# Kernel tuning notes

Measured on AMD Instinct MI355X. Metric: run time of the kernel, lower is better.

Reference implementation:

```python
import jax, jax.numpy as jnp
import numpy as np

EMB = 1024
HEADS = 16
HEAD_DIM = EMB // HEADS
FF = 4 * EMB
EPS = 1e-5


def setup_inputs() -> dict:
    key = jax.random.key(0)
    ks = jax.random.split(key, 16)
    s = 0.02
    return {
        "x": jax.random.normal(ks[0], (2, 2048, EMB), dtype=jnp.float32),
        "ln1_g": jnp.ones((EMB,), jnp.float32),
        "ln1_b": jnp.zeros((EMB,), jnp.float32),
        "Wq": jax.random.normal(ks[1], (EMB, EMB), jnp.float32) * s,
        "bq": jnp.zeros((EMB,), jnp.float32),
        "Wk": jax.random.normal(ks[2], (EMB, EMB), jnp.float32) * s,
        "bk": jnp.zeros((EMB,), jnp.float32),
        "Wv": jax.random.normal(ks[3], (EMB, EMB), jnp.float32) * s,
        "bv": jnp.zeros((EMB,), jnp.float32),
        "Wo": jax.random.normal(ks[4], (EMB, EMB), jnp.float32) * s,
        "bo": jnp.zeros((EMB,), jnp.float32),
        "ln2_g": jnp.ones((EMB,), jnp.float32),
        "ln2_b": jnp.zeros((EMB,), jnp.float32),
        "W1": jax.random.normal(ks[5], (EMB, FF), jnp.float32) * s,
        "b1": jnp.zeros((FF,), jnp.float32),
        "W2": jax.random.normal(ks[6], (FF, EMB), jnp.float32) * s,
        "b2": jnp.zeros((EMB,), jnp.float32),
    }


def _layernorm(x, g, b):
    mu = jnp.mean(x, axis=-1, keepdims=True)
    var = jnp.var(x, axis=-1, keepdims=True)
    return (x - mu) * jax.lax.rsqrt(var + EPS) * g + b


def _attention(x, Wq, bq, Wk, bk, Wv, bv, Wo, bo):
    B, T, C = x.shape
    # [B,T,C] -> [B,H,T,Dh]
    def split(y):
        return y.reshape(B, T, HEADS, HEAD_DIM).transpose(0, 2, 1, 3)
    Q = split(x @ Wq + bq)
    K = split(x @ Wk + bk)
    V = split(x @ Wv + bv)
    att = jnp.einsum("bhqd,bhkd->bhqk", Q, K) / np.sqrt(HEAD_DIM).astype(np.float32)
    causal = jnp.tril(jnp.ones((T, T), bool))
    att = jnp.where(causal, att, -jnp.inf)
    att = jax.nn.softmax(att, axis=-1)
    out = jnp.einsum("bhqk,bhkd->bhqd", att, V)
    out = out.transpose(0, 2, 1, 3).reshape(B, T, C)
    return out @ Wo + bo


def reference(x, ln1_g, ln1_b, Wq, bq, Wk, bk, Wv, bv, Wo, bo,
              ln2_g, ln2_b, W1, b1, W2, b2):
    # dropout is identity in eval mode
    x = x + _attention(_layernorm(x, ln1_g, ln1_b), Wq, bq, Wk, bk, Wv, bv, Wo, bo)
    h = _layernorm(x, ln2_g, ln2_b)
    h = jax.nn.gelu(h @ W1 + b1, approximate=False) @ W2 + b2
    return x + h
```

## Files before the change

### kernel.cpp

```cpp
#include <hip/hip_runtime.h>
#include <hip/hip_bf16.h>

typedef __attribute__((ext_vector_type(4))) float f32x4;
typedef __attribute__((ext_vector_type(8))) short bf16x8;
typedef unsigned int u32;
typedef unsigned short u16;

#define GASP __attribute__((address_space(1)))
#define LASP __attribute__((address_space(3)))

__device__ __forceinline__ u16 f2bf(float f) {
  u32 u = __float_as_uint(f);
  return (u16)((u + 0x7fffu + ((u >> 16) & 1u)) >> 16);
}

__device__ __forceinline__ u32 cvtpk(float lo, float hi) {
  u32 r;
  asm("v_cvt_pk_bf16_f32 %0, %1, %2" : "=v"(r) : "v"(lo), "v"(hi));
  return r;
}

__device__ __forceinline__ void gl_lds16(const void* g, void* l) {
  __builtin_amdgcn_global_load_lds((const GASP u32*)g, (LASP u32*)l, 16, 0, 0);
}

struct CastArgs {
  const float* s[6];
  u16* d[6];
};

__global__ __launch_bounds__(256) void cast_w(CastArgs a) {
  int bid = blockIdx.x;
  int w, t, K, N, kshift;
  if (bid < 4096)      { w = bid >> 10; t = bid & 1023; K = 1024; N = 1024; kshift = 5; }
  else if (bid < 8192) { w = 4; t = bid - 4096; K = 1024; N = 4096; kshift = 5; }
  else                 { w = 5; t = bid - 8192; K = 4096; N = 1024; kshift = 7; }
  int tk = t & ((1 << kshift) - 1);
  int tn = t >> kshift;
  int k0 = tk << 5, n0 = tn << 5;
  const float* src = a.s[w];
  u16* dst = a.d[w];
  __shared__ u16 tile[32][36];
  int r = threadIdx.x >> 3, c0 = (threadIdx.x & 7) << 2;
  float4 v = *(const float4*)&src[(size_t)(k0 + r) * N + n0 + c0];
  tile[c0 + 0][r] = f2bf(v.x);
  tile[c0 + 1][r] = f2bf(v.y);
  tile[c0 + 2][r] = f2bf(v.z);
  tile[c0 + 3][r] = f2bf(v.w);
  __syncthreads();
  ushort4 o;
  o.x = tile[r][c0 + 0];
  o.y = tile[r][c0 + 1];
  o.z = tile[r][c0 + 2];
  o.w = tile[r][c0 + 3];
  *(ushort4*)&dst[(size_t)(n0 + r) * K + k0 + c0] = o;
}

__global__ __launch_bounds__(256) void ln_k(const float* __restrict__ x, const float* __restrict__ g,
                                            const float* __restrict__ b, u16* __restrict__ out) {
  int row = blockIdx.x;
  int tid = threadIdx.x;
  float4 v = *(const float4*)&x[(size_t)row * 1024 + tid * 4];
  float s = v.x + v.y + v.z + v.w;
  float ss = v.x * v.x + v.y * v.y + v.z * v.z + v.w * v.w;
#pragma unroll
  for (int o = 32; o >= 1; o >>= 1) {
    s += __shfl_xor(s, o, 64);
    ss += __shfl_xor(ss, o, 64);
  }
  __shared__ float red[8];
  int wv = tid >> 6;
  if ((tid & 63) == 0) { red[wv] = s; red[wv + 4] = ss; }
  __syncthreads();
  s = red[0] + red[1] + red[2] + red[3];
  ss = red[4] + red[5] + red[6] + red[7];
  float mu = s * (1.0f / 1024.0f);
  float var = ss * (1.0f / 1024.0f) - mu * mu;
  float rstd = rsqrtf(var + 1e-5f);
  float4 gv = *(const float4*)&g[tid * 4];
  float4 bv = *(const float4*)&b[tid * 4];
  ushort4 o4;
  o4.x = f2bf((v.x - mu) * rstd * gv.x + bv.x);
  o4.y = f2bf((v.y - mu) * rstd * gv.y + bv.y);
  o4.z = f2bf((v.z - mu) * rstd * gv.z + bv.z);
  o4.w = f2bf((v.w - mu) * rstd * gv.w + bv.w);
  *(ushort4*)&out[(size_t)row * 1024 + tid * 4] = o4;
}

template <int MODE>
__global__ __launch_bounds__(512, 2) void gemm_256(
    const u16* __restrict__ A, const u16* __restrict__ Bt,
    const float* __restrict__ bias0, const float* __restrict__ bias1, const float* __restrict__ bias2,
    void* outp, int rm, int rn, int xn, int M, int N, int K) {
  __shared__ __align__(16) u16 As[4][128 * 64];
  __shared__ __align__(16) u16 Bs[4][128 * 64];
  char* asB = (char*)As;
  char* bsB = (char*)Bs;
  const int tid = threadIdx.x;
  const int w = tid >> 6, lane = tid & 63;
  const int xcd = blockIdx.x & 7, idx = blockIdx.x >> 3;
  const int mt = (xcd / xn) * rm + (idx % rm);
  const int nt = (xcd % xn) * rn + (idx / rm);
  const int m0 = mt << 8, n0 = nt << 8;

  const int rA = tid >> 3;
  const int csw = ((tid & 7) ^ (rA & 7)) * 8;
  const u16* pA = A + (size_t)(m0 + rA) * K + csw;
  const u16* pB = Bt + (size_t)(n0 + rA) * K + csw;
  const int dstOff = tid * 16;

#define STG_A(kt, h, d_) do {                                            \
    const u16* s_ = pA + (size_t)((h) * 128) * K + (size_t)(kt) * 64;    \
    char* l_ = asB + ((d_) * 2 + (h)) * 16384 + dstOff;                  \
    gl_lds16(s_, l_);                                                    \
    gl_lds16(s_ + (size_t)64 * K, l_ + 8192);                            \
  } while (0)
#define STG_B(kt, h, d_) do {                                            \
    const u16* s_ = pB + (size_t)((h) * 128) * K + (size_t)(kt) * 64;    \
    char* l_ = bsB + ((d_) * 2 + (h)) * 16384 + dstOff;                  \
    gl_lds16(s_, l_);                                                    \
    gl_lds16(s_ + (size_t)64 * K, l_ + 8192);                            \
  } while (0)

  const int wr = w >> 2, wc = w & 3;
  const int g = lane >> 4, qi = lane & 15;

  int aOff[8][2], bOff[4][2];
#pragma unroll
  for (int mm = 0; mm < 8; ++mm) {
    int row = mm * 16 + qi;
#pragma unroll
    for (int ks = 0; ks < 2; ++ks)
      aOff[mm][ks] = row * 128 + (((ks * 4 + g) ^ (qi & 7)) << 4);
  }
#pragma unroll
  for (int nn = 0; nn < 4; ++nn) {
    int rowb = (wc & 1) * 64 + nn * 16 + qi;
#pragma unroll
    for (int ks = 0; ks < 2; ++ks)
      bOff[nn][ks] = rowb * 128 + (((ks * 4 + g) ^ (qi & 7)) << 4);
  }

  f32x4 acc[8][4];
#pragma unroll
  for (int i = 0; i < 8; ++i)
#pragma unroll
    for (int j = 0; j < 4; ++j) acc[i][j] = f32x4{0.f, 0.f, 0.f, 0.f};

#define MFMA16(MB, A00, A01, A10, A11) do {                                              \
    __builtin_amdgcn_s_setprio(1);                                                       \
    acc[(MB)][0] = __builtin_amdgcn_mfma_f32_16x16x32_bf16(A00, bv[0][0], acc[(MB)][0], 0, 0, 0); \
    acc[(MB)][1] = __builtin_amdgcn_mfma_f32_16x16x32_bf16(A00, bv[1][0], acc[(MB)][1], 0, 0, 0); \
    acc[(MB)][2] = __builtin_amdgcn_mfma_f32_16x16x32_bf16(A00, bv[2][0], acc[(MB)][2], 0, 0, 0); \
    acc[(MB)][3] = __builtin_amdgcn_mfma_f32_16x16x32_bf16(A00, bv[3][0], acc[(MB)][3], 0, 0, 0); \
    acc[(MB) + 1][0] = __builtin_amdgcn_mfma_f32_16x16x32_bf16(A10, bv[0][0], acc[(MB) + 1][0], 0, 0, 0); \
    acc[(MB) + 1][1] = __builtin_amdgcn_mfma_f32_16x16x32_bf16(A10, bv[1][0], acc[(MB) + 1][1], 0, 0, 0); \
    acc[(MB) + 1][2] = __builtin_amdgcn_mfma_f32_16x16x32_bf16(A10, bv[2][0], acc[(MB) + 1][2], 0, 0, 0); \
    acc[(MB) + 1][3] = __builtin_amdgcn_mfma_f32_16x16x32_bf16(A10, bv[3][0], acc[(MB) + 1][3], 0, 0, 0); \
    acc[(MB)][0] = __builtin_amdgcn_mfma_f32_16x16x32_bf16(A01, bv[0][1], acc[(MB)][0], 0, 0, 0); \
    acc[(MB)][1] = __builtin_amdgcn_mfma_f32_16x16x32_bf16(A01, bv[1][1], acc[(MB)][1], 0, 0, 0); \
    acc[(MB)][2] = __builtin_amdgcn_mfma_f32_16x16x32_bf16(A01, bv[2][1], acc[(MB)][2], 0, 0, 0); \
    acc[(MB)][3] = __builtin_amdgcn_mfma_f32_16x16x32_bf16(A01, bv[3][1], acc[(MB)][3], 0, 0, 0); \
    acc[(MB) + 1][0] = __builtin_amdgcn_mfma_f32_16x16x32_bf16(A11, bv[0][1], acc[(MB) + 1][0], 0, 0, 0); \
    acc[(MB) + 1][1] = __builtin_amdgcn_mfma_f32_16x16x32_bf16(A11, bv[1][1], acc[(MB) + 1][1], 0, 0, 0); \
    acc[(MB) + 1][2] = __builtin_amdgcn_mfma_f32_16x16x32_bf16(A11, bv[2][1], acc[(MB) + 1][2], 0, 0, 0); \
    acc[(MB) + 1][3] = __builtin_amdgcn_mfma_f32_16x16x32_bf16(A11, bv[3][1], acc[(MB) + 1][3], 0, 0, 0); \
    __builtin_amdgcn_s_setprio(0);                                                       \
  } while (0)

#define RDA(dst0, dst1, MB)                                          \
    bf16x8 dst0##0 = *(const bf16x8*)(asB + aTB + aOff[(MB)][0]);     \
    bf16x8 dst0##1 = *(const bf16x8*)(asB + aTB + aOff[(MB)][1]);     \
    bf16x8 dst1##0 = *(const bf16x8*)(asB + aTB + aOff[(MB) + 1][0]); \
    bf16x8 dst1##1 = *(const bf16x8*)(asB + aTB + aOff[(MB) + 1][1]);

  const int T = K >> 6;
  STG_A(0, 0, 0); STG_A(0, 1, 0);
  STG_B(0, 0, 0); STG_B(0, 1, 0);
  asm volatile("s_waitcnt vmcnt(0)" ::: "memory");
  __builtin_amdgcn_s_barrier();

  for (int t = 0; t < T; ++t) {
    const int d = t & 1;
    const int aTB = (d * 2 + wr) * 16384;
    const int bTB = (d * 2 + (wc >> 1)) * 16384;
    bf16x8 bv[4][2];
#pragma unroll
    for (int nn = 0; nn < 4; ++nn) {
      bv[nn][0] = *(const bf16x8*)(bsB + bTB + bOff[nn][0]);
      bv[nn][1] = *(const bf16x8*)(bsB + bTB + bOff[nn][1]);
    }
    RDA(p0a, p0b, 0);
    if (t + 1 < T) STG_A(t + 1, 0, d ^ 1);
    MFMA16(0, p0a0, p0a1, p0b0, p0b1);
    RDA(p1a, p1b, 2);
    if (t + 1 < T) STG_A(t + 1, 1, d ^ 1);
    MFMA16(2, p1a0, p1a1, p1b0, p1b1);
    RDA(p2a, p2b, 4);
    if (t + 1 < T) STG_B(t + 1, 0, d ^ 1);
    MFMA16(4, p2a0, p2a1, p2b0, p2b1);
    RDA(p3a, p3b, 6);
    if (t + 1 < T) STG_B(t + 1, 1, d ^ 1);
    MFMA16(6, p3a0, p3a1, p3b0, p3b1);
    asm volatile("" ::: "memory");
    if (t + 1 < T) { asm volatile("s_waitcnt vmcnt(0)" ::: "memory"); }
    __builtin_amdgcn_s_barrier();
  }
#undef MFMA16
#undef RDA
#undef STG_A
#undef STG_B

  const int ci = lane & 15;
#pragma unroll
  for (int mm = 0; mm < 8; ++mm) {
#pragma unroll
    for (int nn = 0; nn < 4; ++nn) {
      int colb = n0 + wc * 64 + nn * 16 + ci;
      int rowbase = m0 + wr * 128 + mm * 16 + 4 * g;
      f32x4 c = acc[mm][nn];
      if constexpr (MODE == 2) {
        int sel = colb >> 10;
        int cc = colb & 1023;
        const float* bp = sel == 0 ? bias0 : (sel == 1 ? bias1 : bias2);
        float bb = bp[cc];
        int h = cc >> 6, dd = cc & 63;
        int b_ = rowbase >> 11, tt = rowbase & 2047;
        if (sel == 2) {
          u16* op = (u16*)outp + 2ull * (4096ull * 1024ull);
          ushort4 o4;
          o4.x = f2bf(c[0] + bb);
          o4.y = f2bf(c[1] + bb);
          o4.z = f2bf(c[2] + bb);
          o4.w = f2bf(c[3] + bb);
          *(ushort4*)&op[((size_t)(b_ * 16 + h) * 64 + dd) * 2048 + tt] = o4;
        } else {
          float scale = (sel == 0) ? 0.125f : 1.0f;
          u16* op = (u16*)outp + (size_t)sel * (4096ull * 1024ull);
#pragma unroll
          for (int r = 0; r < 4; ++r)
            op[((size_t)(b_ * 16 + h) * 2048 + tt + r) * 64 + dd] = f2bf((c[r] + bb) * scale);
        }
      } else {
        float bb = bias0[colb];
#pragma unroll
        for (int r = 0; r < 4; ++r) {
          float v = c[r] + bb;
          float gl = 0.5f * v * (1.0f + erff(v * 0.70710678118654752f));
          ((u16*)outp)[(size_t)(rowbase + r) * N + colb] = f2bf(gl);
        }
      }
    }
  }
}

__global__ __launch_bounds__(512) void gemm_sk(
    const u16* __restrict__ A, const u16* __restrict__ Bt,
    const float* __restrict__ bias0, float* __restrict__ outp,
    const float* __restrict__ res, int M, int N, int K) {
  __shared__ __align__(16) union SM {
    struct { u16 As[2][4][128 * 32]; u16 Bs[2][4][128 * 32]; } t;
    float red[16][4][4][64];
  } sm;
  const int tid = threadIdx.x;
  const int w8 = tid >> 6, lane = tid & 63;
  const int gg = w8 >> 2, wl = w8 & 3;
  const int m0 = blockIdx.y << 7, n0 = blockIdx.x << 7;

  char* asB = (char*)sm.t.As[gg];
  char* bsB = (char*)sm.t.Bs[gg];
  const u16* aS[2];
  const u16* bS[2];
#pragma unroll
  for (int i = 0; i < 2; ++i) {
    int p = wl * 2048 + i * 1024 + lane * 16;
    int r = p >> 6;
    int cl = ((p >> 4) & 3) ^ ((r >> 1) & 3);
    aS[i] = A + (size_t)(m0 + r) * K + gg * 32 + cl * 8;
    bS[i] = Bt + (size_t)(n0 + r) * K + gg * 32 + cl * 8;
  }
  f32x4 acc[4][4];
#pragma unroll
  for (int i = 0; i < 4; ++i)
#pragma unroll
    for (int j = 0; j < 4; ++j) acc[i][j] = f32x4{0.f, 0.f, 0.f, 0.f};

  const int wr = wl >> 1, wc = wl & 1;
  int aOff[4], bOff[4];
#pragma unroll
  for (int mm = 0; mm < 4; ++mm) {
    int rowa = wr * 64 + mm * 16 + (lane & 15);
    aOff[mm] = rowa * 64 + (((lane >> 4) ^ ((rowa >> 1) & 3)) << 4);
    int rowb = wc * 64 + mm * 16 + (lane & 15);
    bOff[mm] = rowb * 64 + (((lane >> 4) ^ ((rowb >> 1) & 3)) << 4);
  }

  gl_lds16(aS[0], asB + wl * 2048);
  gl_lds16(aS[1], asB + wl * 2048 + 1024);
  gl_lds16(bS[0], bsB + wl * 2048);
  gl_lds16(bS[1], bsB + wl * 2048 + 1024);
  if (K > 64) {
    gl_lds16(aS[0] + 64, asB + 8192 + wl * 2048);
    gl_lds16(aS[1] + 64, asB + 8192 + wl * 2048 + 1024);
    gl_lds16(bS[0] + 64, bsB + 8192 + wl * 2048);
    gl_lds16(bS[1] + 64, bsB + 8192 + wl * 2048 + 1024);
  }
  if (K > 128) {
    gl_lds16(aS[0] + 128, asB + 16384 + wl * 2048);
    gl_lds16(aS[1] + 128, asB + 16384 + wl * 2048 + 1024);
    gl_lds16(bS[0] + 128, bsB + 16384 + wl * 2048);
    gl_lds16(bS[1] + 128, bsB + 16384 + wl * 2048 + 1024);
  }
  int buf = 0;
  for (int ks = 0; ks < K; ks += 64) {
    const int rem = ((K - ks) >> 6) - 1;
    if (rem >= 2)      { asm volatile("s_waitcnt vmcnt(8)" ::: "memory"); }
    else if (rem == 1) { asm volatile("s_waitcnt vmcnt(4)" ::: "memory"); }
    else               { asm volatile("s_waitcnt vmcnt(0)" ::: "memory"); }
    __builtin_amdgcn_s_barrier();
    asm volatile("" ::: "memory");
    if (ks + 192 < K) {
      const int nb = ((buf + 3) & 3) * 8192;
      gl_lds16(aS[0] + ks + 192, asB + nb + wl * 2048);
      gl_lds16(aS[1] + ks + 192, asB + nb + wl * 2048 + 1024);
      gl_lds16(bS[0] + ks + 192, bsB + nb + wl * 2048);
      gl_lds16(bS[1] + ks + 192, bsB + nb + wl * 2048 + 1024);
    }
    const int tb = buf * 8192;
    bf16x8 av[4], bv[4];
#pragma unroll
    for (int mm = 0; mm < 4; ++mm) av[mm] = *(const bf16x8*)(asB + tb + aOff[mm]);
#pragma unroll
    for (int nn = 0; nn < 4; ++nn) bv[nn] = *(const bf16x8*)(bsB + tb + bOff[nn]);
#pragma unroll
    for (int mm = 0; mm < 4; ++mm)
#pragma unroll
      for (int nn = 0; nn < 4; ++nn)
        acc[mm][nn] = __builtin_amdgcn_mfma_f32_16x16x32_bf16(av[mm], bv[nn], acc[mm][nn], 0, 0, 0);
    buf = (buf + 1) & 3;
  }

  __syncthreads();
  if (gg == 1) {
#pragma unroll
    for (int mm = 0; mm < 4; ++mm)
#pragma unroll
      for (int nn = 0; nn < 4; ++nn)
#pragma unroll
        for (int r = 0; r < 4; ++r) sm.red[mm * 4 + nn][r][wl][lane] = acc[mm][nn][r];
  }
  __syncthreads();
  if (gg == 0) {
    const int g = lane >> 4, ci = lane & 15;
#pragma unroll
    for (int mm = 0; mm < 4; ++mm) {
#pragma unroll
      for (int nn = 0; nn < 4; ++nn) {
        int colb = n0 + wc * 64 + nn * 16 + ci;
        int rowbase = m0 + wr * 64 + mm * 16 + 4 * g;
        float bb = bias0[colb];
#pragma unroll
        for (int r = 0; r < 4; ++r) {
          size_t idx = (size_t)(rowbase + r) * N + colb;
          outp[idx] = acc[mm][nn][r] + sm.red[mm * 4 + nn][r][wl][lane] + bb + res[idx];
        }
      }
    }
  }
}

__global__ __launch_bounds__(512) void attn_k(const u16* __restrict__ Q, const u16* __restrict__ Kg,
                                              const u16* __restrict__ Vt, u16* __restrict__ O) {
  __shared__ __align__(16) u16 Ks[2][4][64 * 64];
  __shared__ __align__(16) u16 Vs[2][4][64 * 64];
  const int bx = blockIdx.y;
  const int bh = blockIdx.x;
  const int tid = threadIdx.x, w = tid >> 6, lane = tid & 63;
  const int g = lane >> 4, qi = lane & 15;
  const u16* Qb = Q + (size_t)bh * 2048 * 64;
  const u16* Kb = Kg + (size_t)bh * 2048 * 64;
  const u16* Vtb = Vt + (size_t)bh * 64 * 2048;

  const int rS = tid >> 3, cS = tid & 7;
  const int csw = (cS ^ (rS & 7)) * 8;
  const u16* srcK = Kb + (size_t)rS * 64 + csw;
  const u16* srcV = Vtb + (size_t)rS * 2048 + csw;
  char* ksB = (char*)Ks;
  char* vsB = (char*)Vs;
  const int dstOff = tid * 16;

  int koff[4][2], voff[4][2];
#pragma unroll
  for (int t = 0; t < 4; ++t) {
    int row = 16 * t + qi;
#pragma unroll
    for (int h = 0; h < 2; ++h) koff[t][h] = row * 128 + (((4 * h + g) ^ (qi & 7)) << 4);
#pragma unroll
    for (int kt = 0; kt < 2; ++kt) voff[t][kt] = row * 128 + (((4 * kt + g) ^ (qi & 7)) << 4);
  }

  const int b_ = bh >> 4, hh = bh & 15;
  u32* Ou = (u32*)O;

  for (int job = 0; job < 2; ++job) {
    const int qt = job ? bx : 15 - bx;
    const int qmin = qt * 128 + w * 16;
    const int qrow = qmin + qi;
    const int qmaxw = qmin + 15;

    bf16x8 qf[2];
#pragma unroll
    for (int h = 0; h < 2; ++h)
      qf[h] = *(const bf16x8*)(Qb + (size_t)qrow * 64 + h * 32 + g * 8);

    f32x4 acc[4];
#pragma unroll
    for (int dt = 0; dt < 4; ++dt) acc[dt] = f32x4{0.f, 0.f, 0.f, 0.f};
    float m = -1e30f, lsum = 0.0f;

    __syncthreads();
#pragma unroll
    for (int j = 0; j < 4; ++j) {
      gl_lds16(srcK + (size_t)j * 4096, ksB + j * 8192 + dstOff);
      gl_lds16(srcV + (size_t)j * 64, vsB + j * 8192 + dstOff);
    }

    const int nsteps = 2 * qt + 2;
    const int quads = (nsteps + 3) >> 2;
    int ph = 0;
    for (int ss = 0; ss < quads; ++ss) {
      __syncthreads();
      if (ss + 1 < quads) {
        const int nb = (ph ^ 1) * 32768;
#pragma unroll
        for (int j = 0; j < 4; ++j) {
          const int sj = 4 * ss + 4 + j;
          gl_lds16(srcK + (size_t)sj * 4096, ksB + nb + j * 8192 + dstOff);
          gl_lds16(srcV + (size_t)sj * 64, vsB + nb + j * 8192 + dstOff);
        }
      }
#pragma unroll
      for (int j = 0; j < 4; ++j) {
        const int s = 4 * ss + j;
        const int kv0 = s * 64;
        if (kv0 <= qmaxw) {
          const int tb = ph * 32768 + j * 8192;
          f32x4 st[4];
          __builtin_amdgcn_s_setprio(1);
#pragma unroll
          for (int t = 0; t < 4; ++t) {
            st[t] = f32x4{0.f, 0.f, 0.f, 0.f};
#pragma unroll
            for (int h = 0; h < 2; ++h) {
              bf16x8 kf = *(const bf16x8*)(ksB + tb + koff[t][h]);
              st[t] = __builtin_amdgcn_mfma_f32_16x16x32_bf16(kf, qf[h], st[t], 0, 0, 0);
            }
          }
          __builtin_amdgcn_s_setprio(0);
          float pvv[4][4];
          float tmax = -1e30f;
          if (kv0 + 63 > qmin) {
#pragma unroll
            for (int t = 0; t < 4; ++t)
#pragma unroll
              for (int r = 0; r < 4; ++r) {
                int key = kv0 + 16 * t + 4 * g + r;
                float sv = st[t][r];
                sv = (key <= qrow) ? sv : -1e30f;
                pvv[t][r] = sv;
                tmax = fmaxf(tmax, sv);
              }
          } else {
#pragma unroll
            for (int t = 0; t < 4; ++t)
#pragma unroll
              for (int r = 0; r < 4; ++r) {
                float sv = st[t][r];
                pvv[t][r] = sv;
                tmax = fmaxf(tmax, sv);
              }
          }
          tmax = fmaxf(tmax, __shfl_xor(tmax, 16, 64));
          tmax = fmaxf(tmax, __shfl_xor(tmax, 32, 64));
          if (!__all(tmax <= m + 8.0f)) {
            float mn = fmaxf(m, tmax);
            float corr = __expf(m - mn);
            lsum *= corr;
#pragma unroll
            for (int dt = 0; dt < 4; ++dt)
#pragma unroll
              for (int r = 0; r < 4; ++r) acc[dt][r] *= corr;
            m = mn;
          }
          float tsum = 0.f;
#pragma unroll
          for (int t = 0; t < 4; ++t)
#pragma unroll
            for (int r = 0; r < 4; ++r) {
              float e = __expf(pvv[t][r] - m);
              pvv[t][r] = e;
              tsum += e;
            }
          tsum += __shfl_xor(tsum, 16, 64);
          tsum += __shfl_xor(tsum, 32, 64);
          lsum += tsum;
          u32 pk[4][2], ex[4][2];
#pragma unroll
          for (int t = 0; t < 4; ++t)
#pragma unroll
            for (int p = 0; p < 2; ++p) {
              u32 v = cvtpk(pvv[t][2 * p], pvv[t][2 * p + 1]);
              pk[t][p] = v;
              ex[t][p] = (u32)__shfl_xor((int)v, 16, 64);
            }
          const bool ge = (g & 1) == 0;
          const bool G0 = (g >> 1) == 0;
          const bool innr = (g == 0) || (g == 3);
          u32 mm_[4][4];
#pragma unroll
          for (int t = 0; t < 4; ++t) {
            mm_[t][0] = ge ? pk[t][0] : ex[t][0];
            mm_[t][1] = ge ? pk[t][1] : ex[t][1];
            mm_[t][2] = ge ? ex[t][0] : pk[t][0];
            mm_[t][3] = ge ? ex[t][1] : pk[t][1];
          }
          union Frag { u32 u[4]; bf16x8 v; } f0, f1;
#pragma unroll
          for (int i = 0; i < 4; ++i) {
            u32 sel0 = G0 ? mm_[1][i] : mm_[0][i];
            u32 sel1 = G0 ? mm_[3][i] : mm_[2][i];
            u32 sw0 = (u32)__shfl_xor((int)sel0, 32, 64);
            u32 sw1 = (u32)__shfl_xor((int)sel1, 32, 64);
            u32 own0 = G0 ? mm_[0][i] : mm_[1][i];
            u32 own1 = G0 ? mm_[2][i] : mm_[3][i];
            f0.u[i] = innr ? own0 : sw0;
            f1.u[i] = innr ? own1 : sw1;
          }
          __builtin_amdgcn_s_setprio(1);
#pragma unroll
          for (int dt = 0; dt < 4; ++dt) {
            bf16x8 vfa = *(const bf16x8*)(vsB + tb + voff[dt][0]);
            acc[dt] = __builtin_amdgcn_mfma_f32_16x16x32_bf16(vfa, f0.v, acc[dt], 0, 0, 0);
            bf16x8 vfb = *(const bf16x8*)(vsB + tb + voff[dt][1]);
            acc[dt] = __builtin_amdgcn_mfma_f32_16x16x32_bf16(vfb, f1.v, acc[dt], 0, 0, 0);
          }
          __builtin_amdgcn_s_setprio(0);
        }
      }
      ph ^= 1;
    }

    float rl = 1.0f / lsum;
    size_t rowq = (size_t)(b_ * 2048 + qrow);
#pragma unroll
    for (int dt = 0; dt < 4; ++dt) {
#pragma unroll
      for (int rp = 0; rp < 2; ++rp) {
        u16 lo = f2bf(acc[dt][rp * 2] * rl);
        u16 hi = f2bf(acc[dt][rp * 2 + 1] * rl);
        u32 pkd = (u32)lo | ((u32)hi << 16);
        size_t off = rowq * 1024 + hh * 64 + dt * 16 + 4 * g + rp * 2;
        Ou[off >> 1] = pkd;
      }
    }
  }
}

extern "C" void kernel_launch(void* const* d_in, const int* in_sizes, int n_in,
                              void* d_out, int out_size, void* d_ws, size_t ws_size,
                              hipStream_t stream) {
  const float* x    = (const float*)d_in[0];
  const float* ln1g = (const float*)d_in[1];
  const float* ln1b = (const float*)d_in[2];
  const float* Wq   = (const float*)d_in[3];
  const float* bq   = (const float*)d_in[4];
  const float* Wk   = (const float*)d_in[5];
  const float* bk   = (const float*)d_in[6];
  const float* Wv   = (const float*)d_in[7];
  const float* bv   = (const float*)d_in[8];
  const float* Wo   = (const float*)d_in[9];
  const float* bo   = (const float*)d_in[10];
  const float* ln2g = (const float*)d_in[11];
  const float* ln2b = (const float*)d_in[12];
  const float* W1   = (const float*)d_in[13];
  const float* b1   = (const float*)d_in[14];
  const float* W2   = (const float*)d_in[15];
  const float* b2   = (const float*)d_in[16];

  char* ws = (char*)d_ws;
  const size_t MB = 1ull << 20;
  u16* WqT = (u16*)(ws + 0 * MB);
  u16* WkT = (u16*)(ws + 2 * MB);
  u16* WvT = (u16*)(ws + 4 * MB);
  u16* WoT = (u16*)(ws + 6 * MB);
  u16* W1T = (u16*)(ws + 8 * MB);
  u16* W2T = (u16*)(ws + 16 * MB);
  u16* XN  = (u16*)(ws + 24 * MB);
  u16* Qb  = (u16*)(ws + 32 * MB);
  u16* Kb  = (u16*)(ws + 40 * MB);
  u16* Vtb = (u16*)(ws + 48 * MB);
  u16* Ob  = (u16*)(ws + 56 * MB);
  u16* Gb  = (u16*)(ws + 32 * MB);

  CastArgs ca;
  ca.s[0] = Wq; ca.s[1] = Wk; ca.s[2] = Wv; ca.s[3] = Wo; ca.s[4] = W1; ca.s[5] = W2;
  ca.d[0] = WqT; ca.d[1] = WkT; ca.d[2] = WvT; ca.d[3] = WoT; ca.d[4] = W1T; ca.d[5] = W2T;
  cast_w<<<12288, 256, 0, stream>>>(ca);

  ln_k<<<4096, 256, 0, stream>>>(x, ln1g, ln1b, XN);

  gemm_256<2><<<192, 512, 0, stream>>>(XN, WqT, bq, bk, bv, Qb, 4, 6, 2, 4096, 3072, 1024);

  attn_k<<<dim3(32, 8), 512, 0, stream>>>(Qb, Kb, Vtb, Ob);

  gemm_sk<<<dim3(8, 32), 512, 0, stream>>>(Ob, WoT, bo, (float*)d_out, x, 4096, 1024, 1024);

  ln_k<<<4096, 256, 0, stream>>>((const float*)d_out, ln2g, ln2b, XN);

  gemm_256<3><<<256, 512, 0, stream>>>(XN, W1T, b1, nullptr, nullptr, Gb, 8, 4, 4, 4096, 4096, 1024);

  gemm_sk<<<dim3(8, 32), 512, 0, stream>>>(Gb, W2T, b2, (float*)d_out, (const float*)d_out, 4096, 1024, 4096);
}
```

Baseline: 226.8 us.

## Template GEMM on N-tile width, use 256x192 tiles for QKV projection

The 256-wide GEMM is parameterized on the N tile width, with a simpler LDS layout and warp-to-column mapping (each warp covers BN/4 columns). The QKV projection now uses 256x192 tiles, launching 256 blocks instead of 192, which better fills the GPU's compute units (256 on MI355X) and balances across XCDs. The trade-off is less B-tile reuse per block, and the warp mapping changes for the FFN GEMM too.

```diff
diff --git a/kernel.cpp b/kernel.cpp
--- a/kernel.cpp
+++ b/kernel.cpp
@@ -87,13 +87,15 @@
   *(ushort4*)&out[(size_t)row * 1024 + tid * 4] = o4;
 }
 
-template <int MODE>
+template <int MODE, int BN>
 __global__ __launch_bounds__(512, 2) void gemm_256(
     const u16* __restrict__ A, const u16* __restrict__ Bt,
     const float* __restrict__ bias0, const float* __restrict__ bias1, const float* __restrict__ bias2,
     void* outp, int rm, int rn, int xn, int M, int N, int K) {
-  __shared__ __align__(16) u16 As[4][128 * 64];
-  __shared__ __align__(16) u16 Bs[4][128 * 64];
+  constexpr int NN = BN / 64;
+  constexpr int BB = BN * 128;
+  __shared__ __align__(16) u16 As[2][256 * 64];
+  __shared__ __align__(16) u16 Bs[2][BN * 64];
   char* asB = (char*)As;
   char* bsB = (char*)Bs;
   const int tid = threadIdx.x;
@@ -101,7 +103,7 @@
   const int xcd = blockIdx.x & 7, idx = blockIdx.x >> 3;
   const int mt = (xcd / xn) * rm + (idx % rm);
   const int nt = (xcd % xn) * rn + (idx / rm);
-  const int m0 = mt << 8, n0 = nt << 8;
+  const int m0 = mt << 8, n0 = nt * BN;
 
   const int rA = tid >> 3;
   const int csw = ((tid & 7) ^ (rA & 7)) * 8;
@@ -109,62 +111,46 @@
   const u16* pB = Bt + (size_t)(n0 + rA) * K + csw;
   const int dstOff = tid * 16;
 
-#define STG_A(kt, h, d_) do {                                            \
-    const u16* s_ = pA + (size_t)((h) * 128) * K + (size_t)(kt) * 64;    \
-    char* l_ = asB + ((d_) * 2 + (h)) * 16384 + dstOff;                  \
-    gl_lds16(s_, l_);                                                    \
-    gl_lds16(s_ + (size_t)64 * K, l_ + 8192);                            \
-  } while (0)
-#define STG_B(kt, h, d_) do {                                            \
-    const u16* s_ = pB + (size_t)((h) * 128) * K + (size_t)(kt) * 64;    \
-    char* l_ = bsB + ((d_) * 2 + (h)) * 16384 + dstOff;                  \
-    gl_lds16(s_, l_);                                                    \
-    gl_lds16(s_ + (size_t)64 * K, l_ + 8192);                            \
-  } while (0)
+#define STG_A(kt, j) gl_lds16(pA + (size_t)((j) * 64) * K + (size_t)(kt) * 64, asB + aNB + (j) * 8192 + dstOff)
+#define STG_B(kt, j) gl_lds16(pB + (size_t)((j) * 64) * K + (size_t)(kt) * 64, bsB + bNB + (j) * 8192 + dstOff)
 
   const int wr = w >> 2, wc = w & 3;
   const int g = lane >> 4, qi = lane & 15;
 
-  int aOff[8][2], bOff[4][2];
+  int aOff[8][2], bOff[NN][2];
 #pragma unroll
   for (int mm = 0; mm < 8; ++mm) {
-    int row = mm * 16 + qi;
+    int row = wr * 128 + mm * 16 + qi;
 #pragma unroll
     for (int ks = 0; ks < 2; ++ks)
       aOff[mm][ks] = row * 128 + (((ks * 4 + g) ^ (qi & 7)) << 4);
   }
 #pragma unroll
-  for (int nn = 0; nn < 4; ++nn) {
-    int rowb = (wc & 1) * 64 + nn * 16 + qi;
+  for (int nn = 0; nn < NN; ++nn) {
+    int rowb = wc * (BN / 4) + nn * 16 + qi;
 #pragma unroll
     for (int ks = 0; ks < 2; ++ks)
       bOff[nn][ks] = rowb * 128 + (((ks * 4 + g) ^ (qi & 7)) << 4);
   }
 
-  f32x4 acc[8][4];
+  f32x4 acc[8][NN];
 #pragma unroll
   for (int i = 0; i < 8; ++i)
 #pragma unroll
-    for (int j = 0; j < 4; ++j) acc[i][j] = f32x4{0.f, 0.f, 0.f, 0.f};
-
-#define MFMA16(MB, A00, A01, A10, A11) do {                                              \
+    for (int j = 0; j < NN; ++j) acc[i][j] = f32x4{0.f, 0.f, 0.f, 0.f};
+
+#define PAIR(MB, A00, A01, A10, A11) do {                                                \
     __builtin_amdgcn_s_setprio(1);                                                       \
-    acc[(MB)][0] = __builtin_amdgcn_mfma_f32_16x16x32_bf16(A00, bv[0][0], acc[(MB)][0], 0, 0, 0); \
-    acc[(MB)][1] = __builtin_amdgcn_mfma_f32_16x16x32_bf16(A00, bv[1][0], acc[(MB)][1], 0, 0, 0); \
-    acc[(MB)][2] = __builtin_amdgcn_mfma_f32_16x16x32_bf16(A00, bv[2][0], acc[(MB)][2], 0, 0, 0); \
-    acc[(MB)][3] = __builtin_amdgcn_mfma_f32_16x16x32_bf16(A00, bv[3][0], acc[(MB)][3], 0, 0, 0); \
-    acc[(MB) + 1][0] = __builtin_amdgcn_mfma_f32_16x16x32_bf16(A10, bv[0][0], acc[(MB) + 1][0], 0, 0, 0); \
-    acc[(MB) + 1][1] = __builtin_amdgcn_mfma_f32_16x16x32_bf16(A10, bv[1][0], acc[(MB) + 1][1], 0, 0, 0); \
-    acc[(MB) + 1][2] = __builtin_amdgcn_mfma_f32_16x16x32_bf16(A10, bv[2][0], acc[(MB) + 1][2], 0, 0, 0); \
-    acc[(MB) + 1][3] = __builtin_amdgcn_mfma_f32_16x16x32_bf16(A10, bv[3][0], acc[(MB) + 1][3], 0, 0, 0); \
-    acc[(MB)][0] = __builtin_amdgcn_mfma_f32_16x16x32_bf16(A01, bv[0][1], acc[(MB)][0], 0, 0, 0); \
-    acc[(MB)][1] = __builtin_amdgcn_mfma_f32_16x16x32_bf16(A01, bv[1][1], acc[(MB)][1], 0, 0, 0); \
-    acc[(MB)][2] = __builtin_amdgcn_mfma_f32_16x16x32_bf16(A01, bv[2][1], acc[(MB)][2], 0, 0, 0); \
-    acc[(MB)][3] = __builtin_amdgcn_mfma_f32_16x16x32_bf16(A01, bv[3][1], acc[(MB)][3], 0, 0, 0); \
-    acc[(MB) + 1][0] = __builtin_amdgcn_mfma_f32_16x16x32_bf16(A11, bv[0][1], acc[(MB) + 1][0], 0, 0, 0); \
-    acc[(MB) + 1][1] = __builtin_amdgcn_mfma_f32_16x16x32_bf16(A11, bv[1][1], acc[(MB) + 1][1], 0, 0, 0); \
-    acc[(MB) + 1][2] = __builtin_amdgcn_mfma_f32_16x16x32_bf16(A11, bv[2][1], acc[(MB) + 1][2], 0, 0, 0); \
-    acc[(MB) + 1][3] = __builtin_amdgcn_mfma_f32_16x16x32_bf16(A11, bv[3][1], acc[(MB) + 1][3], 0, 0, 0); \
+    _Pragma("unroll")                                                                    \
+    for (int nn = 0; nn < NN; ++nn) {                                                    \
+      acc[(MB)][nn] = __builtin_amdgcn_mfma_f32_16x16x32_bf16(A00, bv[nn][0], acc[(MB)][nn], 0, 0, 0);         \
+      acc[(MB) + 1][nn] = __builtin_amdgcn_mfma_f32_16x16x32_bf16(A10, bv[nn][0], acc[(MB) + 1][nn], 0, 0, 0); \
+    }                                                                                    \
+    _Pragma("unroll")                                                                    \
+    for (int nn = 0; nn < NN; ++nn) {                                                    \
+      acc[(MB)][nn] = __builtin_amdgcn_mfma_f32_16x16x32_bf16(A01, bv[nn][1], acc[(MB)][nn], 0, 0, 0);         \
+      acc[(MB) + 1][nn] = __builtin_amdgcn_mfma_f32_16x16x32_bf16(A11, bv[nn][1], acc[(MB) + 1][nn], 0, 0, 0); \
+    }                                                                                    \
     __builtin_amdgcn_s_setprio(0);                                                       \
   } while (0)
 
@@ -175,38 +161,45 @@
     bf16x8 dst1##1 = *(const bf16x8*)(asB + aTB + aOff[(MB) + 1][1]);
 
   const int T = K >> 6;
-  STG_A(0, 0, 0); STG_A(0, 1, 0);
-  STG_B(0, 0, 0); STG_B(0, 1, 0);
+#pragma unroll
+  for (int j = 0; j < 4; ++j) gl_lds16(pA + (size_t)(j * 64) * K, asB + j * 8192 + dstOff);
+#pragma unroll
+  for (int j = 0; j < NN; ++j) gl_lds16(pB + (size_t)(j * 64) * K, bsB + j * 8192 + dstOff);
   asm volatile("s_waitcnt vmcnt(0)" ::: "memory");
   __builtin_amdgcn_s_barrier();
 
   for (int t = 0; t < T; ++t) {
     const int d = t & 1;
-    const int aTB = (d * 2 + wr) * 16384;
-    const int bTB = (d * 2 + (wc >> 1)) * 16384;
-    bf16x8 bv[4][2];
-#pragma unroll
-    for (int nn = 0; nn < 4; ++nn) {
+    const int aTB = d * 32768, bTB = d * BB;
+    const int aNB = (d ^ 1) * 32768, bNB = (d ^ 1) * BB;
+    const bool more = (t + 1 < T);
+    const int kt1 = t + 1;
+    bf16x8 bv[NN][2];
+#pragma unroll
+    for (int nn = 0; nn < NN; ++nn) {
       bv[nn][0] = *(const bf16x8*)(bsB + bTB + bOff[nn][0]);
       bv[nn][1] = *(const bf16x8*)(bsB + bTB + bOff[nn][1]);
     }
     RDA(p0a, p0b, 0);
-    if (t + 1 < T) STG_A(t + 1, 0, d ^ 1);
-    MFMA16(0, p0a0, p0a1, p0b0, p0b1);
+    if (more) { STG_A(kt1, 0); STG_A(kt1, 1); }
+    PAIR(0, p0a0, p0a1, p0b0, p0b1);
     RDA(p1a, p1b, 2);
-    if (t + 1 < T) STG_A(t + 1, 1, d ^ 1);
-    MFMA16(2, p1a0, p1a1, p1b0, p1b1);
+    if (more) { STG_A(kt1, 2); STG_A(kt1, 3); }
+    PAIR(2, p1a0, p1a1, p1b0, p1b1);
     RDA(p2a, p2b, 4);
-    if (t + 1 < T) STG_B(t + 1, 0, d ^ 1);
-    MFMA16(4, p2a0, p2a1, p2b0, p2b1);
+    if (more) { STG_B(kt1, 0); STG_B(kt1, 1); }
+    PAIR(4, p2a0, p2a1, p2b0, p2b1);
     RDA(p3a, p3b, 6);
-    if (t + 1 < T) STG_B(t + 1, 1, d ^ 1);
-    MFMA16(6, p3a0, p3a1, p3b0, p3b1);
+    if (more) {
+#pragma unroll
+      for (int j = 2; j < NN; ++j) STG_B(kt1, j);
+    }
+    PAIR(6, p3a0, p3a1, p3b0, p3b1);
     asm volatile("" ::: "memory");
-    if (t + 1 < T) { asm volatile("s_waitcnt vmcnt(0)" ::: "memory"); }
+    if (more) { asm volatile("s_waitcnt vmcnt(0)" ::: "memory"); }
     __builtin_amdgcn_s_barrier();
   }
-#undef MFMA16
+#undef PAIR
 #undef RDA
 #undef STG_A
 #undef STG_B
@@ -215,8 +208,8 @@
 #pragma unroll
   for (int mm = 0; mm < 8; ++mm) {
 #pragma unroll
-    for (int nn = 0; nn < 4; ++nn) {
-      int colb = n0 + wc * 64 + nn * 16 + ci;
+    for (int nn = 0; nn < NN; ++nn) {
+      int colb = n0 + wc * (BN / 4) + nn * 16 + ci;
       int rowbase = m0 + wr * 128 + mm * 16 + 4 * g;
       f32x4 c = acc[mm][nn];
       if constexpr (MODE == 2) {
@@ -609,7 +602,7 @@
 
   ln_k<<<4096, 256, 0, stream>>>(x, ln1g, ln1b, XN);
 
-  gemm_256<2><<<192, 512, 0, stream>>>(XN, WqT, bq, bk, bv, Qb, 4, 6, 2, 4096, 3072, 1024);
+  gemm_256<2, 192><<<256, 512, 0, stream>>>(XN, WqT, bq, bk, bv, Qb, 8, 4, 4, 4096, 3072, 1024);
 
   attn_k<<<dim3(32, 8), 512, 0, stream>>>(Qb, Kb, Vtb, Ob);
 
@@ -617,7 +610,7 @@
 
   ln_k<<<4096, 256, 0, stream>>>((const float*)d_out, ln2g, ln2b, XN);
 
-  gemm_256<3><<<256, 512, 0, stream>>>(XN, W1T, b1, nullptr, nullptr, Gb, 8, 4, 4, 4096, 4096, 1024);
+  gemm_256<3, 256><<<256, 512, 0, stream>>>(XN, W1T, b1, nullptr, nullptr, Gb, 8, 4, 4, 4096, 4096, 1024);
 
   gemm_sk<<<dim3(8, 32), 512, 0, stream>>>(Gb, W2T, b2, (float*)d_out, (const float*)d_out, 4096, 1024, 4096);
 }
```

Measured after the change: 223.8 us. Within noise of the previous version (-1.3%).
